# Kernel optimization log

Measured on AMD Instinct MI355X. Metric: run time of the kernel, lower is better.

The kernel has to match this reference:

```python
import jax, jax.numpy as jnp
import numpy as np

N_NODES = 100000


def sage_conv(x, src, dst, counts, Wl, bl, Wr):
    # mean-aggregate source features into destination nodes
    msg_sum = jax.ops.segment_sum(x[src], dst, num_segments=N_NODES)  # [N, d]
    aggr = msg_sum / counts  # zero-degree nodes stay 0 (counts clamped to 1)
    return aggr @ Wl + bl + x @ Wr


def setup_inputs() -> dict:
    key = jax.random.key(0)
    ks = jax.random.split(key, 16)
    N, E, IN, H, OUT = N_NODES, 640000, 128, 128, 40
    x = jax.random.normal(ks[0], (N, IN), dtype=jnp.float32)
    edge_index = jax.random.randint(ks[1], (2, E), 0, N, dtype=jnp.int64)

    def lin(k, fan_in, fan_out):
        s = 1.0 / np.sqrt(fan_in)
        return jax.random.uniform(k, (fan_in, fan_out), jnp.float32, -s, s)

    return {
        "x": x,
        "edge_index": edge_index,
        "W1l": lin(ks[2], IN, H), "b1": jnp.zeros((H,), jnp.float32), "W1r": lin(ks[3], IN, H),
        "W2l": lin(ks[4], H, H), "b2": jnp.zeros((H,), jnp.float32), "W2r": lin(ks[5], H, H),
        "W3l": lin(ks[6], H, H), "b3": jnp.zeros((H,), jnp.float32), "W3r": lin(ks[7], H, H),
        "Wf1": lin(ks[8], H, H), "bf1": jnp.zeros((H,), jnp.float32),
        "Wf2": lin(ks[9], H, OUT), "bf2": jnp.zeros((OUT,), jnp.float32),
    }


def reference(x, edge_index, W1l, b1, W1r, W2l, b2, W2r, W3l, b3, W3r, Wf1, bf1, Wf2, bf2):
    src, dst = edge_index[0], edge_index[1]
    counts = jax.ops.segment_sum(jnp.ones_like(dst, dtype=x.dtype), dst,
                                 num_segments=N_NODES)
    counts = jnp.maximum(counts, 1.0)[:, None]  # [N, 1]

    h = jax.nn.relu(sage_conv(x, src, dst, counts, W1l, b1, W1r))
    h = jax.nn.relu(sage_conv(h, src, dst, counts, W2l, b2, W2r))
    h = sage_conv(h, src, dst, counts, W3l, b3, W3r)

    z = jax.nn.relu(h @ Wf1 + bf1) @ Wf2 + bf2  # [N, out]
    return jax.nn.log_softmax(z, axis=1), h
```

## Files before the change

kernel.cpp:

```cpp
#include <hip/hip_runtime.h>
#include <math.h>

#define N_NODES 100000
#define HDIM    128
#define ODIM    40
#define NBLK    ((N_NODES + 255) / 256)

typedef unsigned short u16;
typedef unsigned int   u32;
typedef short bf16x8 __attribute__((ext_vector_type(8)));
typedef float f32x4  __attribute__((ext_vector_type(4)));

__device__ inline float bf16lo_to_f(u32 v) {
    u32 u = v << 16; float f; __builtin_memcpy(&f, &u, 4); return f;
}
__device__ inline float bf16hi_to_f(u32 v) {
    u32 u = v & 0xffff0000u; float f; __builtin_memcpy(&f, &u, 4); return f;
}
__device__ inline u16 f_to_bf16(float f) {
    u32 u; __builtin_memcpy(&u, &f, 4);
    u32 r = (u + 0x7fffu + ((u >> 16) & 1u)) >> 16;
    return (u16)r;
}
__device__ inline u32 pack_bf16x2(float a, float b) {
    return (u32)f_to_bf16(a) | ((u32)f_to_bf16(b) << 16);
}

__global__ __launch_bounds__(256) void count_deg_kernel(
    const int* __restrict__ dst, int* __restrict__ ic, int E)
{
    int e = blockIdx.x * 256 + threadIdx.x;
    if (e < E) atomicAdd(ic + dst[e], 1);
}

__global__ __launch_bounds__(256) void block_sum_kernel(
    const int* __restrict__ ic, int* __restrict__ bs, int n)
{
    __shared__ int sm[256];
    int t = threadIdx.x;
    int i = blockIdx.x * 256 + t;
    sm[t] = (i < n) ? ic[i] : 0;
    __syncthreads();
    for (int s = 128; s > 0; s >>= 1) {
        if (t < s) sm[t] += sm[t + s];
        __syncthreads();
    }
    if (t == 0) bs[blockIdx.x] = sm[0];
}

__global__ __launch_bounds__(512) void scan_bs_kernel(int* __restrict__ bs, int nb)
{
    __shared__ int sm[512];
    int t = threadIdx.x;
    sm[t] = (t < nb) ? bs[t] : 0;
    __syncthreads();
    for (int off = 1; off < 512; off <<= 1) {
        int v = (t >= off) ? sm[t - off] : 0;
        __syncthreads();
        sm[t] += v;
        __syncthreads();
    }
    if (t < nb) bs[t] = (t == 0) ? 0 : sm[t - 1];
}

__global__ __launch_bounds__(256) void scan_block_kernel(
    const int* __restrict__ ic, const int* __restrict__ bs,
    int* __restrict__ pc, int n)
{
    __shared__ int sm[256];
    int t = threadIdx.x;
    int i = blockIdx.x * 256 + t;
    int v = (i < n) ? ic[i] : 0;
    sm[t] = v;
    __syncthreads();
    for (int off = 1; off < 256; off <<= 1) {
        int u = (t >= off) ? sm[t - off] : 0;
        __syncthreads();
        sm[t] += u;
        __syncthreads();
    }
    if (i < n) pc[i] = bs[blockIdx.x] + sm[t] - v;
}

__global__ __launch_bounds__(256) void fill_kernel(
    const int* __restrict__ src, const int* __restrict__ dst,
    int* __restrict__ pc, int* __restrict__ cs, int E)
{
    int e = blockIdx.x * 256 + threadIdx.x;
    if (e < E) {
        int p = atomicAdd(pc + dst[e], 1);
        cs[p] = src[e];
    }
}

struct WPtrs { const float* w[7]; };

#define PREP_F2BF  25000
#define PREP_PACKW (PREP_F2BF + 448)
#define PREP_WF2   (PREP_PACKW + 24)
#define PREP_ZERO  (PREP_WF2 + 392)

__global__ __launch_bounds__(256) void prep_kernel(
    const float2* __restrict__ x2, u32* __restrict__ X32,
    WPtrs p, u16* __restrict__ Wpk,
    const float* __restrict__ Wf2, u16* __restrict__ Wf2p,
    int* __restrict__ ic)
{
    const int b = blockIdx.x;
    const int tid = threadIdx.x;
    if (b < PREP_F2BF) {
        int i = b * 256 + tid;
        float2 v = x2[i];
        X32[i] = pack_bf16x2(v.x, v.y);
    } else if (b < PREP_PACKW) {
        int bb = b - PREP_F2BF;
        int mat = bb >> 6;
        int e = (bb & 63) * 256 + tid;
        int k = e >> 7, n = e & 127;
        float v = p.w[mat][e];
        int nt = n >> 4, ks = k >> 5, q = (k >> 3) & 3, j = k & 7;
        Wpk[mat * 16384 + (((nt * 4 + ks) * 64 + q * 16 + (n & 15)) << 3) + j] = f_to_bf16(v);
    } else if (b < PREP_WF2) {
        int e = (b - PREP_PACKW) * 256 + tid;
        if (e < 128 * 48) {
            int k = e / 48, n = e - k * 48;
            float v = (n < ODIM) ? Wf2[k * ODIM + n] : 0.f;
            int nt = n >> 4, ks = k >> 5, q = (k >> 3) & 3, j = k & 7;
            Wf2p[(((nt * 4 + ks) * 64 + q * 16 + (n & 15)) << 3) + j] = f_to_bf16(v);
        }
    } else {
        int i = (b - PREP_WF2) * 256 + tid;
        if (i < 100352) ic[i] = 0;
    }
}

__global__ __launch_bounds__(256) void gather_mean_grp_kernel(
    const u32* __restrict__ feat,
    const int* __restrict__ cs, const int* __restrict__ pc, const int* __restrict__ ic,
    u32* __restrict__ A)
{
    const int grp  = threadIdx.x >> 4;
    const int ch   = threadIdx.x & 15;
    const int node = blockIdx.x * 16 + grp;
    const int end  = pc[node];
    const int deg  = ic[node];
    const int start = end - deg;

    const u32* fb = feat + (ch << 2);

    float acc[8] = {0.f,0.f,0.f,0.f,0.f,0.f,0.f,0.f};
    const uint4 Z = {0u, 0u, 0u, 0u};

    if (deg > 0) {
        uint4 c0 = *reinterpret_cast<const uint4*>(fb + ((size_t)cs[start] << 6));
        uint4 c1 = (deg > 1)
            ? *reinterpret_cast<const uint4*>(fb + ((size_t)cs[start + 1] << 6)) : Z;
        for (int j = 0; j < deg; ++j) {
            uint4 n = (j + 2 < deg)
                ? *reinterpret_cast<const uint4*>(fb + ((size_t)cs[start + j + 2] << 6)) : Z;
            acc[0] += bf16lo_to_f(c0.x); acc[1] += bf16hi_to_f(c0.x);
            acc[2] += bf16lo_to_f(c0.y); acc[3] += bf16hi_to_f(c0.y);
            acc[4] += bf16lo_to_f(c0.z); acc[5] += bf16hi_to_f(c0.z);
            acc[6] += bf16lo_to_f(c0.w); acc[7] += bf16hi_to_f(c0.w);
            c0 = c1; c1 = n;
        }
    }

    float inv = 1.0f / (float)(deg > 0 ? deg : 1);
    uint4 o;
    o.x = pack_bf16x2(acc[0] * inv, acc[1] * inv);
    o.y = pack_bf16x2(acc[2] * inv, acc[3] * inv);
    o.z = pack_bf16x2(acc[4] * inv, acc[5] * inv);
    o.w = pack_bf16x2(acc[6] * inv, acc[7] * inv);
    *reinterpret_cast<uint4*>(A + ((size_t)node << 6) + (ch << 2)) = o;
}

__device__ inline void stage_w(const u16* __restrict__ Wp, u16* __restrict__ sDst,
                               int wave, int lane, int nchunk4)
{
    for (int it = 0; it < nchunk4; ++it) {
        int off = (it * 4 + wave) << 9;
        __builtin_amdgcn_global_load_lds(
            (const __attribute__((address_space(1))) void*)(Wp + off + (lane << 3)),
            (__attribute__((address_space(3))) void*)(sDst + off), 16, 0, 0);
    }
}

__global__ __launch_bounds__(256) void mfma_gemm_kernel(
    const u16* __restrict__ A1, const u16* __restrict__ A2,
    const u16* __restrict__ W1p, const u16* __restrict__ W2p,
    const float* __restrict__ bias,
    u16* __restrict__ out16, float* __restrict__ out32, int do_relu)
{
    __shared__ __align__(16) u16 sBuf[128 * 136];
    const int tid  = threadIdx.x;
    const int wave = tid >> 6;
    const int lane = tid & 63;
    const int m = lane & 15;
    const int q = lane >> 4;
    const int base = blockIdx.x * 128;

    int row0 = base + wave * 16 + m;        if (row0 > N_NODES - 1) row0 = N_NODES - 1;
    int row1 = base + (wave + 4) * 16 + m;  if (row1 > N_NODES - 1) row1 = N_NODES - 1;

    f32x4 acc0[8], acc1[8];
    #pragma unroll
    for (int nt = 0; nt < 8; ++nt) {
        acc0[nt] = (f32x4){0.f, 0.f, 0.f, 0.f};
        acc1[nt] = (f32x4){0.f, 0.f, 0.f, 0.f};
    }

    bf16x8 a0[4], a1[4];
    #pragma unroll
    for (int ks = 0; ks < 4; ++ks) {
        a0[ks] = *reinterpret_cast<const bf16x8*>(A1 + ((size_t)row0 << 7) + ((ks * 4 + q) << 3));
        a1[ks] = *reinterpret_cast<const bf16x8*>(A1 + ((size_t)row1 << 7) + ((ks * 4 + q) << 3));
    }
    stage_w(W1p, sBuf, wave, lane, 8);
    __syncthreads();

    #pragma unroll
    for (int ks = 0; ks < 4; ++ks) {
        #pragma unroll
        for (int nt = 0; nt < 8; ++nt) {
            bf16x8 b = *reinterpret_cast<const bf16x8*>(sBuf + (((nt * 4 + ks) * 64 + lane) << 3));
            acc0[nt] = __builtin_amdgcn_mfma_f32_16x16x32_bf16(a0[ks], b, acc0[nt], 0, 0, 0);
            acc1[nt] = __builtin_amdgcn_mfma_f32_16x16x32_bf16(a1[ks], b, acc1[nt], 0, 0, 0);
        }
    }

    if (A2 != nullptr) {
        __syncthreads();
        #pragma unroll
        for (int ks = 0; ks < 4; ++ks) {
            a0[ks] = *reinterpret_cast<const bf16x8*>(A2 + ((size_t)row0 << 7) + ((ks * 4 + q) << 3));
            a1[ks] = *reinterpret_cast<const bf16x8*>(A2 + ((size_t)row1 << 7) + ((ks * 4 + q) << 3));
        }
        stage_w(W2p, sBuf, wave, lane, 8);
        __syncthreads();

        #pragma unroll
        for (int ks = 0; ks < 4; ++ks) {
            #pragma unroll
            for (int nt = 0; nt < 8; ++nt) {
                bf16x8 b = *reinterpret_cast<const bf16x8*>(sBuf + (((nt * 4 + ks) * 64 + lane) << 3));
                acc0[nt] = __builtin_amdgcn_mfma_f32_16x16x32_bf16(a0[ks], b, acc0[nt], 0, 0, 0);
                acc1[nt] = __builtin_amdgcn_mfma_f32_16x16x32_bf16(a1[ks], b, acc1[nt], 0, 0, 0);
            }
        }
    }
    __syncthreads();

    #pragma unroll
    for (int nt = 0; nt < 8; ++nt) {
        int col = nt * 16 + m;
        float bv = bias[col];
        #pragma unroll
        for (int r = 0; r < 4; ++r) {
            float v0 = acc0[nt][r] + bv;
            float v1 = acc1[nt][r] + bv;
            if (do_relu) { v0 = fmaxf(v0, 0.f); v1 = fmaxf(v1, 0.f); }
            int rl0 = wave * 16 + q * 4 + r;
            int rl1 = rl0 + 64;
            sBuf[rl0 * 136 + col] = f_to_bf16(v0);
            sBuf[rl1 * 136 + col] = f_to_bf16(v1);
            if (out32) {
                int rg0 = base + rl0, rg1 = base + rl1;
                if (rg0 < N_NODES) out32[((size_t)rg0 << 7) + col] = v0;
                if (rg1 < N_NODES) out32[((size_t)rg1 << 7) + col] = v1;
            }
        }
    }
    __syncthreads();

    if (out16) {
        #pragma unroll
        for (int it = 0; it < 8; ++it) {
            int c = it * 256 + tid;
            int row = c >> 4, ch = c & 15;
            int rowg = base + row;
            if (rowg < N_NODES)
                *reinterpret_cast<uint4*>(out16 + ((size_t)rowg << 7) + (ch << 3)) =
                    *reinterpret_cast<const uint4*>(sBuf + row * 136 + (ch << 3));
        }
    }
}

__global__ __launch_bounds__(256) void mfma_head_kernel(
    const u16* __restrict__ h3,
    const u16* __restrict__ Wf1p, const float* __restrict__ bf1,
    const u16* __restrict__ Wf2p, const float* __restrict__ bf2,
    float* __restrict__ out)
{
    __shared__ __align__(16) u16 sW1[16384];
    __shared__ __align__(16) u16 sW2[6144];
    const int tid  = threadIdx.x;
    const int wave = tid >> 6;
    const int lane = tid & 63;
    const int m = lane & 15;
    const int q = lane >> 4;
    const int base = blockIdx.x * 128;

    int row0 = base + wave * 16 + m;       if (row0 > N_NODES - 1) row0 = N_NODES - 1;
    int row1 = base + 64 + wave * 16 + m;  if (row1 > N_NODES - 1) row1 = N_NODES - 1;

    bf16x8 a0[4], a1[4];
    #pragma unroll
    for (int ks = 0; ks < 4; ++ks) {
        a0[ks] = *reinterpret_cast<const bf16x8*>(h3 + ((size_t)row0 << 7) + ((ks * 4 + q) << 3));
        a1[ks] = *reinterpret_cast<const bf16x8*>(h3 + ((size_t)row1 << 7) + ((ks * 4 + q) << 3));
    }
    stage_w(Wf1p, sW1, wave, lane, 8);
    stage_w(Wf2p, sW2, wave, lane, 3);
    __syncthreads();

    f32x4 acc0[8], acc1[8];
    #pragma unroll
    for (int nt = 0; nt < 8; ++nt) {
        acc0[nt] = (f32x4){0.f, 0.f, 0.f, 0.f};
        acc1[nt] = (f32x4){0.f, 0.f, 0.f, 0.f};
    }
    #pragma unroll
    for (int ks = 0; ks < 4; ++ks) {
        #pragma unroll
        for (int nt = 0; nt < 8; ++nt) {
            bf16x8 b = *reinterpret_cast<const bf16x8*>(sW1 + (((nt * 4 + ks) * 64 + lane) << 3));
            acc0[nt] = __builtin_amdgcn_mfma_f32_16x16x32_bf16(a0[ks], b, acc0[nt], 0, 0, 0);
            acc1[nt] = __builtin_amdgcn_mfma_f32_16x16x32_bf16(a1[ks], b, acc1[nt], 0, 0, 0);
        }
    }
    __syncthreads();

    #pragma unroll
    for (int nt = 0; nt < 8; ++nt) {
        int col = nt * 16 + m;
        float bv = bf1[col];
        #pragma unroll
        for (int r = 0; r < 4; ++r) {
            int dc = (wave * 4 + (nt >> 1)) * 64 + ((nt & 1) * 2 + (m >> 3)) * 16 + (q * 4 + r);
            sW1[(dc << 3) | (m & 7)]        = f_to_bf16(fmaxf(acc0[nt][r] + bv, 0.f));
            sW1[8192 + ((dc << 3) | (m & 7))] = f_to_bf16(fmaxf(acc1[nt][r] + bv, 0.f));
        }
    }
    __syncthreads();

    f32x4 ca[3], cb[3];
    #pragma unroll
    for (int nt = 0; nt < 3; ++nt) {
        ca[nt] = (f32x4){0.f, 0.f, 0.f, 0.f};
        cb[nt] = (f32x4){0.f, 0.f, 0.f, 0.f};
    }
    #pragma unroll
    for (int ks = 0; ks < 4; ++ks) {
        bf16x8 t0 = *reinterpret_cast<const bf16x8*>(sW1 + (((wave * 4 + ks) * 64 + lane) << 3));
        bf16x8 t1 = *reinterpret_cast<const bf16x8*>(sW1 + 8192 + (((wave * 4 + ks) * 64 + lane) << 3));
        #pragma unroll
        for (int nt = 0; nt < 3; ++nt) {
            bf16x8 b = *reinterpret_cast<const bf16x8*>(sW2 + (((nt * 4 + ks) * 64 + lane) << 3));
            ca[nt] = __builtin_amdgcn_mfma_f32_16x16x32_bf16(t0, b, ca[nt], 0, 0, 0);
            cb[nt] = __builtin_amdgcn_mfma_f32_16x16x32_bf16(t1, b, cb[nt], 0, 0, 0);
        }
    }

    #pragma unroll
    for (int tile = 0; tile < 2; ++tile) {
        const f32x4* acc2 = tile ? cb : ca;
        float z[3][4];
        float mx[4] = {-INFINITY, -INFINITY, -INFINITY, -INFINITY};
        #pragma unroll
        for (int nt = 0; nt < 3; ++nt) {
            int col = nt * 16 + m;
            bool valid = (col < ODIM);
            float bv = valid ? bf2[col] : 0.f;
            #pragma unroll
            for (int r = 0; r < 4; ++r) {
                z[nt][r] = acc2[nt][r] + bv;
                if (valid) mx[r] = fmaxf(mx[r], z[nt][r]);
            }
        }
        #pragma unroll
        for (int off = 1; off < 16; off <<= 1) {
            #pragma unroll
            for (int r = 0; r < 4; ++r) mx[r] = fmaxf(mx[r], __shfl_xor(mx[r], off, 16));
        }
        float sum[4] = {0.f, 0.f, 0.f, 0.f};
        #pragma unroll
        for (int nt = 0; nt < 3; ++nt) {
            int col = nt * 16 + m;
            if (col < ODIM) {
                #pragma unroll
                for (int r = 0; r < 4; ++r) sum[r] += expf(z[nt][r] - mx[r]);
            }
        }
        #pragma unroll
        for (int off = 1; off < 16; off <<= 1) {
            #pragma unroll
            for (int r = 0; r < 4; ++r) sum[r] += __shfl_xor(sum[r], off, 16);
        }
        float lse[4];
        #pragma unroll
        for (int r = 0; r < 4; ++r) lse[r] = logf(sum[r]) + mx[r];

        int rowbase = base + tile * 64 + wave * 16;
        #pragma unroll
        for (int nt = 0; nt < 3; ++nt) {
            int col = nt * 16 + m;
            if (col >= ODIM) continue;
            #pragma unroll
            for (int r = 0; r < 4; ++r) {
                int rowg = rowbase + q * 4 + r;
                if (rowg < N_NODES) out[(size_t)rowg * ODIM + col] = z[nt][r] - lse[r];
            }
        }
    }
}

extern "C" void kernel_launch(void* const* d_in, const int* in_sizes, int n_in,
                              void* d_out, int out_size, void* d_ws, size_t ws_size,
                              hipStream_t stream) {
    const float* x   = (const float*)d_in[0];
    const int*   ei  = (const int*)d_in[1];
    const int E = in_sizes[1] / 2;
    const int* src = ei;
    const int* dst = ei + E;

    const float* W1l = (const float*)d_in[2];
    const float* b1  = (const float*)d_in[3];
    const float* W1r = (const float*)d_in[4];
    const float* W2l = (const float*)d_in[5];
    const float* b2  = (const float*)d_in[6];
    const float* W2r = (const float*)d_in[7];
    const float* W3l = (const float*)d_in[8];
    const float* b3  = (const float*)d_in[9];
    const float* W3r = (const float*)d_in[10];
    const float* Wf1 = (const float*)d_in[11];
    const float* bf1 = (const float*)d_in[12];
    const float* Wf2 = (const float*)d_in[13];
    const float* bf2 = (const float*)d_in[14];

    float* out     = (float*)d_out;
    float* outTail = out + (size_t)N_NODES * ODIM;

    int* ic = (int*)out;
    int* pc = ic + 100352;
    int* bs = pc + 100352;
    int* cs = bs + 1024;

    const size_t FEAT16 = (size_t)N_NODES * HDIM;
    u16* X16  = (u16*)d_ws;
    u16* F16a = X16  + FEAT16;
    u16* F16b = F16a + FEAT16;
    u16* A16  = F16b + FEAT16;
    u16* Wpk  = A16  + FEAT16;
    u16* Wp_1l = Wpk + 0 * 16384;
    u16* Wp_1r = Wpk + 1 * 16384;
    u16* Wp_2l = Wpk + 2 * 16384;
    u16* Wp_2r = Wpk + 3 * 16384;
    u16* Wp_3l = Wpk + 4 * 16384;
    u16* Wp_3r = Wpk + 5 * 16384;
    u16* Wp_f1 = Wpk + 6 * 16384;
    u16* Wf2p  = Wpk + 7 * 16384;

    const int gemmGrid   = (N_NODES + 127) / 128;
    const int gatherGrid = N_NODES / 16;
    const int edgeGrid   = (E + 255) / 256;

    WPtrs wp; wp.w[0] = W1l; wp.w[1] = W1r; wp.w[2] = W2l; wp.w[3] = W2r;
    wp.w[4] = W3l; wp.w[5] = W3r; wp.w[6] = Wf1;
    prep_kernel<<<PREP_ZERO, 256, 0, stream>>>(
        (const float2*)x, (u32*)X16, wp, Wpk, Wf2, Wf2p, ic);

    count_deg_kernel<<<edgeGrid, 256, 0, stream>>>(dst, ic, E);
    block_sum_kernel<<<NBLK, 256, 0, stream>>>(ic, bs, N_NODES);
    scan_bs_kernel<<<1, 512, 0, stream>>>(bs, NBLK);
    scan_block_kernel<<<NBLK, 256, 0, stream>>>(ic, bs, pc, N_NODES);
    fill_kernel<<<edgeGrid, 256, 0, stream>>>(src, dst, pc, cs, E);

    gather_mean_grp_kernel<<<gatherGrid, 256, 0, stream>>>((const u32*)X16, cs, pc, ic, (u32*)A16);
    mfma_gemm_kernel<<<gemmGrid, 256, 0, stream>>>(A16, X16, Wp_1l, Wp_1r, b1, F16a, nullptr, 1);

    gather_mean_grp_kernel<<<gatherGrid, 256, 0, stream>>>((const u32*)F16a, cs, pc, ic, (u32*)A16);
    mfma_gemm_kernel<<<gemmGrid, 256, 0, stream>>>(A16, F16a, Wp_2l, Wp_2r, b2, F16b, nullptr, 1);

    gather_mean_grp_kernel<<<gatherGrid, 256, 0, stream>>>((const u32*)F16b, cs, pc, ic, (u32*)A16);
    mfma_gemm_kernel<<<gemmGrid, 256, 0, stream>>>(A16, F16b, Wp_3l, Wp_3r, b3, F16a, outTail, 0);

    mfma_head_kernel<<<gemmGrid, 256, 0, stream>>>(F16a, Wp_f1, bf1, Wf2p, bf2, out);
}
```

Measured before the change: 398.7 us.

## Restructure SAGE GEMM to 512 threads with both weights staged upfront

The dense SAGE layer GEMM now runs 8 waves per 128-row block, one 16-row tile per wave, instead of 4 waves handling two tiles each. Both weight matrices are loaded into a 64KB LDS buffer at once, and both A operands are loaded into registers up front, which removes the second staging phase and its extra barrier. This halves accumulator registers per thread and raises the wave count, but the larger LDS footprint may cap how many blocks fit per CU.

New measurement: 389.8 us, median of 2. -2.2%, faster.

```diff
diff --git a/kernel.cpp b/kernel.cpp
--- a/kernel.cpp
+++ b/kernel.cpp
@@ -186,13 +186,25 @@
     }
 }
 
-__global__ __launch_bounds__(256) void mfma_gemm_kernel(
+__device__ inline void stage_w8(const u16* __restrict__ Wp, u16* __restrict__ sDst,
+                                int wave, int lane)
+{
+    #pragma unroll
+    for (int it = 0; it < 4; ++it) {
+        int off = (it * 8 + wave) << 9;
+        __builtin_amdgcn_global_load_lds(
+            (const __attribute__((address_space(1))) void*)(Wp + off + (lane << 3)),
+            (__attribute__((address_space(3))) void*)(sDst + off), 16, 0, 0);
+    }
+}
+
+__global__ __launch_bounds__(512) void mfma_gemm_kernel(
     const u16* __restrict__ A1, const u16* __restrict__ A2,
     const u16* __restrict__ W1p, const u16* __restrict__ W2p,
     const float* __restrict__ bias,
     u16* __restrict__ out16, float* __restrict__ out32, int do_relu)
 {
-    __shared__ __align__(16) u16 sBuf[128 * 136];
+    __shared__ __align__(16) u16 sW[32768];
     const int tid  = threadIdx.x;
     const int wave = tid >> 6;
     const int lane = tid & 63;
@@ -200,88 +212,75 @@
     const int q = lane >> 4;
     const int base = blockIdx.x * 128;
 
-    int row0 = base + wave * 16 + m;        if (row0 > N_NODES - 1) row0 = N_NODES - 1;
-    int row1 = base + (wave + 4) * 16 + m;  if (row1 > N_NODES - 1) row1 = N_NODES - 1;
-
-    f32x4 acc0[8], acc1[8];
-    #pragma unroll
-    for (int nt = 0; nt < 8; ++nt) {
-        acc0[nt] = (f32x4){0.f, 0.f, 0.f, 0.f};
-        acc1[nt] = (f32x4){0.f, 0.f, 0.f, 0.f};
-    }
-
-    bf16x8 a0[4], a1[4];
-    #pragma unroll
-    for (int ks = 0; ks < 4; ++ks) {
-        a0[ks] = *reinterpret_cast<const bf16x8*>(A1 + ((size_t)row0 << 7) + ((ks * 4 + q) << 3));
-        a1[ks] = *reinterpret_cast<const bf16x8*>(A1 + ((size_t)row1 << 7) + ((ks * 4 + q) << 3));
-    }
-    stage_w(W1p, sBuf, wave, lane, 8);
-    __syncthreads();
+    int row = base + wave * 16 + m; if (row > N_NODES - 1) row = N_NODES - 1;
+
+    bf16x8 a[4], c[4];
+    #pragma unroll
+    for (int ks = 0; ks < 4; ++ks) {
+        a[ks] = *reinterpret_cast<const bf16x8*>(A1 + ((size_t)row << 7) + ((ks * 4 + q) << 3));
+        c[ks] = *reinterpret_cast<const bf16x8*>(A2 + ((size_t)row << 7) + ((ks * 4 + q) << 3));
+    }
+    stage_w8(W1p, sW, wave, lane);
+    stage_w8(W2p, sW + 16384, wave, lane);
+    __syncthreads();
+
+    f32x4 acc[8];
+    #pragma unroll
+    for (int nt = 0; nt < 8; ++nt) acc[nt] = (f32x4){0.f, 0.f, 0.f, 0.f};
 
     #pragma unroll
     for (int ks = 0; ks < 4; ++ks) {
         #pragma unroll
         for (int nt = 0; nt < 8; ++nt) {
-            bf16x8 b = *reinterpret_cast<const bf16x8*>(sBuf + (((nt * 4 + ks) * 64 + lane) << 3));
-            acc0[nt] = __builtin_amdgcn_mfma_f32_16x16x32_bf16(a0[ks], b, acc0[nt], 0, 0, 0);
-            acc1[nt] = __builtin_amdgcn_mfma_f32_16x16x32_bf16(a1[ks], b, acc1[nt], 0, 0, 0);
-        }
-    }
-
-    if (A2 != nullptr) {
-        __syncthreads();
-        #pragma unroll
-        for (int ks = 0; ks < 4; ++ks) {
-            a0[ks] = *reinterpret_cast<const bf16x8*>(A2 + ((size_t)row0 << 7) + ((ks * 4 + q) << 3));
-            a1[ks] = *reinterpret_cast<const bf16x8*>(A2 + ((size_t)row1 << 7) + ((ks * 4 + q) << 3));
-        }
-        stage_w(W2p, sBuf, wave, lane, 8);
-        __syncthreads();
-
-        #pragma unroll
-        for (int ks = 0; ks < 4; ++ks) {
-            #pragma unroll
-            for (int nt = 0; nt < 8; ++nt) {
-                bf16x8 b = *reinterpret_cast<const bf16x8*>(sBuf + (((nt * 4 + ks) * 64 + lane) << 3));
-                acc0[nt] = __builtin_amdgcn_mfma_f32_16x16x32_bf16(a0[ks], b, acc0[nt], 0, 0, 0);
-                acc1[nt] = __builtin_amdgcn_mfma_f32_16x16x32_bf16(a1[ks], b, acc1[nt], 0, 0, 0);
+            bf16x8 b = *reinterpret_cast<const bf16x8*>(sW + (((nt * 4 + ks) * 64 + lane) << 3));
+            acc[nt] = __builtin_amdgcn_mfma_f32_16x16x32_bf16(a[ks], b, acc[nt], 0, 0, 0);
+        }
+    }
+    #pragma unroll
+    for (int ks = 0; ks < 4; ++ks) {
+        #pragma unroll
+        for (int nt = 0; nt < 8; ++nt) {
+            bf16x8 b = *reinterpret_cast<const bf16x8*>(sW + 16384 + (((nt * 4 + ks) * 64 + lane) << 3));
+            acc[nt] = __builtin_amdgcn_mfma_f32_16x16x32_bf16(c[ks], b, acc[nt], 0, 0, 0);
+        }
+    }
+    __syncthreads();
+
+    if (out32) {
+        #pragma unroll
+        for (int nt = 0; nt < 8; ++nt) {
+            int col = nt * 16 + m;
+            float bv = bias[col];
+            #pragma unroll
+            for (int r = 0; r < 4; ++r) {
+                int rg = base + wave * 16 + q * 4 + r;
+                if (rg < N_NODES) out32[((size_t)rg << 7) + col] = acc[nt][r] + bv;
             }
         }
     }
-    __syncthreads();
-
-    #pragma unroll
-    for (int nt = 0; nt < 8; ++nt) {
-        int col = nt * 16 + m;
-        float bv = bias[col];
-        #pragma unroll
-        for (int r = 0; r < 4; ++r) {
-            float v0 = acc0[nt][r] + bv;
-            float v1 = acc1[nt][r] + bv;
-            if (do_relu) { v0 = fmaxf(v0, 0.f); v1 = fmaxf(v1, 0.f); }
-            int rl0 = wave * 16 + q * 4 + r;
-            int rl1 = rl0 + 64;
-            sBuf[rl0 * 136 + col] = f_to_bf16(v0);
-            sBuf[rl1 * 136 + col] = f_to_bf16(v1);
-            if (out32) {
-                int rg0 = base + rl0, rg1 = base + rl1;
-                if (rg0 < N_NODES) out32[((size_t)rg0 << 7) + col] = v0;
-                if (rg1 < N_NODES) out32[((size_t)rg1 << 7) + col] = v1;
+
+    if (out16) {
+        #pragma unroll
+        for (int nt = 0; nt < 8; ++nt) {
+            int col = nt * 16 + m;
+            float bv = bias[col];
+            #pragma unroll
+            for (int r = 0; r < 4; ++r) {
+                float v = acc[nt][r] + bv;
+                if (do_relu) v = fmaxf(v, 0.f);
+                int rl = wave * 16 + q * 4 + r;
+                sW[rl * 136 + col] = f_to_bf16(v);
             }
         }
-    }
-    __syncthreads();
-
-    if (out16) {
-        #pragma unroll
-        for (int it = 0; it < 8; ++it) {
-            int c = it * 256 + tid;
-            int row = c >> 4, ch = c & 15;
-            int rowg = base + row;
+        __syncthreads();
+        #pragma unroll
+        for (int it = 0; it < 4; ++it) {
+            int cc = it * 512 + tid;
+            int rowl = cc >> 4, ch = cc & 15;
+            int rowg = base + rowl;
             if (rowg < N_NODES)
                 *reinterpret_cast<uint4*>(out16 + ((size_t)rowg << 7) + (ch << 3)) =
-                    *reinterpret_cast<const uint4*>(sBuf + row * 136 + (ch << 3));
+                    *reinterpret_cast<const uint4*>(sW + rowl * 136 + (ch << 3));
         }
     }
 }
@@ -338,7 +337,7 @@
         #pragma unroll
         for (int r = 0; r < 4; ++r) {
             int dc = (wave * 4 + (nt >> 1)) * 64 + ((nt & 1) * 2 + (m >> 3)) * 16 + (q * 4 + r);
-            sW1[(dc << 3) | (m & 7)]        = f_to_bf16(fmaxf(acc0[nt][r] + bv, 0.f));
+            sW1[(dc << 3) | (m & 7)]          = f_to_bf16(fmaxf(acc0[nt][r] + bv, 0.f));
             sW1[8192 + ((dc << 3) | (m & 7))] = f_to_bf16(fmaxf(acc1[nt][r] + bv, 0.f));
         }
     }
@@ -477,13 +476,13 @@
     fill_kernel<<<edgeGrid, 256, 0, stream>>>(src, dst, pc, cs, E);
 
     gather_mean_grp_kernel<<<gatherGrid, 256, 0, stream>>>((const u32*)X16, cs, pc, ic, (u32*)A16);
-    mfma_gemm_kernel<<<gemmGrid, 256, 0, stream>>>(A16, X16, Wp_1l, Wp_1r, b1, F16a, nullptr, 1);
+    mfma_gemm_kernel<<<gemmGrid, 512, 0, stream>>>(A16, X16, Wp_1l, Wp_1r, b1, F16a, nullptr, 1);
 
     gather_mean_grp_kernel<<<gatherGrid, 256, 0, stream>>>((const u32*)F16a, cs, pc, ic, (u32*)A16);
-    mfma_gemm_kernel<<<gemmGrid, 256, 0, stream>>>(A16, F16a, Wp_2l, Wp_2r, b2, F16b, nullptr, 1);
+    mfma_gemm_kernel<<<gemmGrid, 512, 0, stream>>>(A16, F16a, Wp_2l, Wp_2r, b2, F16b, nullptr, 1);
 
     gather_mean_grp_kernel<<<gatherGrid, 256, 0, stream>>>((const u32*)F16b, cs, pc, ic, (u32*)A16);
-    mfma_gemm_kernel<<<gemmGrid, 256, 0, stream>>>(A16, F16b, Wp_3l, Wp_3r, b3, F16a, outTail, 0);
+    mfma_gemm_kernel<<<gemmGrid, 512, 0, stream>>>(A16, F16b, Wp_3l, Wp_3r, b3, F16a, outTail, 0);
 
     mfma_head_kernel<<<gemmGrid, 256, 0, stream>>>(F16a, Wp_f1, bf1, Wf2p, bf2, out);
 }
```
